# Kernel optimization log

Measured on AMD Instinct MI355X. Metric: run time of the kernel, lower is better.

## Reference

```python
import jax, jax.numpy as jnp
import numpy as np

D = 2048    # d_model (feature_dimm)
H = 8       # n_heads
P = 4       # n_points (n_levels = 1)
NL = 4      # num_encoder_layers
DFF = 2048  # dim_feedforward
BS = 2
T = 2048


def setup_inputs() -> dict:
    key = jax.random.key(0)
    ks = jax.random.split(key, 10)
    s = 0.02
    def w(k, shape):
        return jax.random.normal(k, shape, jnp.float32) * s
    return {
        "src": jax.random.normal(ks[0], (BS, D, T), jnp.float32),
        "mask": jnp.ones((BS, T), dtype=bool),
        "level_embed": w(ks[1], (1, D)),
        "Wo": w(ks[2], (NL, D, H * P)), "bo": jnp.zeros((NL, H * P), jnp.float32),
        "Wa": w(ks[3], (NL, D, H * P)), "ba": jnp.zeros((NL, H * P), jnp.float32),
        "Wv": w(ks[4], (NL, D, D)), "bv": jnp.zeros((NL, D), jnp.float32),
        "Wout": w(ks[5], (NL, D, D)), "bout": jnp.zeros((NL, D), jnp.float32),
        "ln1_g": jnp.ones((NL, D), jnp.float32), "ln1_b": jnp.zeros((NL, D), jnp.float32),
        "W1": w(ks[6], (NL, D, DFF)), "b1": jnp.zeros((NL, DFF), jnp.float32),
        "W2": w(ks[7], (NL, DFF, D)), "b2": jnp.zeros((NL, D), jnp.float32),
        "ln2_g": jnp.ones((NL, D), jnp.float32), "ln2_b": jnp.zeros((NL, D), jnp.float32),
    }


def _layer_norm(x, g, b):
    mu = jnp.mean(x, axis=-1, keepdims=True)
    var = jnp.mean((x - mu) ** 2, axis=-1, keepdims=True)
    return (x - mu) * jax.lax.rsqrt(var + 1e-5) * g + b


def _pos_embed_sine(mask, d):
    # 1D PositionEmbeddingSine, normalize=True, temperature=10000
    bs, t = mask.shape
    emb = jnp.cumsum(mask.astype(jnp.float32), axis=1)
    emb = emb / (emb[:, -1:] + 1e-6) * jnp.float32(2.0 * np.pi)
    dim_t = 10000.0 ** (2.0 * (jnp.arange(d) // 2).astype(jnp.float32) / d)
    pos = emb[:, :, None] / dim_t  # (bs, t, d)
    pos = jnp.stack([jnp.sin(pos[..., 0::2]), jnp.cos(pos[..., 1::2])], axis=3)
    return pos.reshape(bs, t, d)


def _deform_attn(q, src, ref, Wv, bv, Wo, bo, Wa, ba, Wout, bout):
    # 1D multi-scale deformable attention, single level.
    bs, Q, d = q.shape
    T_ = src.shape[1]
    dh = d // H
    value = (src @ Wv + bv).reshape(bs, T_, H, dh)
    off = (q @ Wo + bo).reshape(bs, Q, H, P)
    attn = jax.nn.softmax((q @ Wa + ba).reshape(bs, Q, H, P), axis=-1)
    # normalized sampling locations in [0, 1]
    loc = ref[:, :, 0, 0][:, :, None, None] + off / T_  # (bs, Q, H, P)
    x = loc * T_ - 0.5
    i0 = jnp.floor(x)
    w1 = x - i0
    i0i = i0.astype(jnp.int32)
    i1i = i0i + 1
    v0 = ((i0i >= 0) & (i0i < T_)).astype(jnp.float32)  # zero padding
    v1 = ((i1i >= 0) & (i1i < T_)).astype(jnp.float32)
    i0c = jnp.clip(i0i, 0, T_ - 1)
    i1c = jnp.clip(i1i, 0, T_ - 1)
    vh = value.transpose(0, 2, 1, 3)  # (bs, H, T, dh)
    def gather(idx):  # idx: (bs, Q, H, P) -> (bs, H, Q, P, dh)
        idxh = idx.transpose(0, 2, 1, 3).reshape(bs, H, Q * P)
        g = jnp.take_along_axis(vh, idxh[:, :, :, None], axis=2)
        return g.reshape(bs, H, Q, P, dh)
    w0m = ((1.0 - w1) * v0).transpose(0, 2, 1, 3)  # (bs, H, Q, P)
    w1m = (w1 * v1).transpose(0, 2, 1, 3)
    sampled = gather(i0c) * w0m[..., None] + gather(i1c) * w1m[..., None]
    out = jnp.einsum('bhqp,bhqpd->bhqd', attn.transpose(0, 2, 1, 3), sampled)
    out = out.transpose(0, 2, 1, 3).reshape(bs, Q, d)
    return out @ Wout + bout


def reference(src, mask, level_embed, Wo, bo, Wa, ba, Wv, bv, Wout, bout,
              ln1_g, ln1_b, W1, b1, W2, b2, ln2_g, ln2_b):
    bs, c, t = src.shape
    pos = _pos_embed_sine(mask, c)          # (bs, t, c)
    x = src.transpose(0, 2, 1)              # (bs, t, c)
    lvl_pos = pos + level_embed             # (1, c) broadcasts
    vr = jnp.sum(mask.astype(jnp.float32), axis=1) / t  # valid ratios (bs,)
    ref = jnp.linspace(0.5, t - 0.5, t, dtype=jnp.float32)[None] / (vr[:, None] * t)
    ref = (ref * vr[:, None])[:, :, None, None]  # (bs, t, 1, 1)
    for i in range(NL):
        q = x + lvl_pos
        a = _deform_attn(q, x, ref, Wv[i], bv[i], Wo[i], bo[i], Wa[i], ba[i], Wout[i], bout[i])
        x = _layer_norm(x + a, ln1_g[i], ln1_b[i])
        h = jax.nn.relu(x @ W1[i] + b1[i]) @ W2[i] + b2[i]
        x = _layer_norm(x + h, ln2_g[i], ln2_b[i])
    return (x.transpose(0, 2, 1), mask[:, None])
```

## Files before the change

### kernel.cpp

```cpp
#include <hip/hip_runtime.h>

typedef unsigned int u32;
typedef unsigned short u16;
typedef short s8v __attribute__((ext_vector_type(8)));
typedef float f4v __attribute__((ext_vector_type(4)));

#define D_ 2048
#define T_ 2048
#define BS_ 2
#define H_ 8
#define P_ 4
#define NL_ 4
#define DFF_ 2048
#define LDK_ 2048
#define TBUF 24576

#define AS1 __attribute__((address_space(1)))
#define AS3 __attribute__((address_space(3)))

static __device__ __forceinline__ u16 f2bf(float f) {
    u32 u = __float_as_uint(f);
    u = (u + 0x7FFFu + ((u >> 16) & 1u)) >> 16;
    return (u16)u;
}
static __device__ __forceinline__ float bf2f(u16 v) {
    return __uint_as_float(((u32)v) << 16);
}

__global__ void pos_k(const float* __restrict__ le, u16* __restrict__ posbf) {
    int t = blockIdx.x;
    float scale = ((float)(t + 1)) / (2048.0f + 1e-6f) * 6.283185307179586f;
    for (int d = threadIdx.x; d < D_; d += 256) {
        int k = d >> 1;
        float inv_dt = expf(-(float)k * 0.008994473019508361f);
        float th = scale * inv_dt;
        float v = (d & 1) ? cosf(th) : sinf(th);
        posbf[(size_t)t * D_ + d] = f2bf(v + le[d]);
    }
}

__global__ __launch_bounds__(256) void transpose_src_k(const float* __restrict__ src,
                                                       float* __restrict__ x,
                                                       u16* __restrict__ xbf) {
    __shared__ float tile[64][65];
    int b = blockIdx.z;
    int t0 = blockIdx.x * 64, d0 = blockIdx.y * 64;
    const float* s = src + (size_t)b * D_ * T_;
#pragma unroll
    for (int p = 0; p < 16; ++p) {
        int idx = threadIdx.x + p * 256;
        int r = idx >> 6, c = idx & 63;
        tile[r][c] = s[(size_t)(d0 + r) * T_ + t0 + c];
    }
    __syncthreads();
    float* xb = x + (size_t)b * T_ * D_;
    u16* xbb = xbf + (size_t)b * T_ * D_;
#pragma unroll
    for (int p = 0; p < 16; ++p) {
        int idx = threadIdx.x + p * 256;
        int r = idx >> 6, c = idx & 63;
        float v = tile[c][r];
        size_t o = (size_t)(t0 + r) * D_ + d0 + c;
        xb[o] = v;
        xbb[o] = f2bf(v);
    }
}

__global__ __launch_bounds__(256) void transpose_out_k(const float* __restrict__ x,
                                                       float* __restrict__ outp) {
    __shared__ float tile[64][65];
    int b = blockIdx.z;
    int t0 = blockIdx.x * 64, d0 = blockIdx.y * 64;
    const float* xb = x + (size_t)b * T_ * D_;
#pragma unroll
    for (int p = 0; p < 16; ++p) {
        int idx = threadIdx.x + p * 256;
        int r = idx >> 6, c = idx & 63;
        tile[r][c] = xb[(size_t)(t0 + r) * D_ + d0 + c];
    }
    __syncthreads();
    float* ob = outp + (size_t)b * D_ * T_;
#pragma unroll
    for (int p = 0; p < 16; ++p) {
        int idx = threadIdx.x + p * 256;
        int r = idx >> 6, c = idx & 63;
        ob[(size_t)(d0 + r) * T_ + t0 + c] = tile[c][r];
    }
}

__global__ void mask_out_k(float* __restrict__ outp) {
    int i = blockIdx.x * 256 + threadIdx.x;
    if (i < BS_ * T_) outp[i] = 1.0f;
}

__global__ __launch_bounds__(256) void transpose_cvt4_k(const float* __restrict__ Wv,
                                                        const float* __restrict__ Wout,
                                                        const float* __restrict__ W1,
                                                        const float* __restrict__ W2,
                                                        u16* __restrict__ WtV,
                                                        u16* __restrict__ Wt1,
                                                        u16* __restrict__ Wt2,
                                                        u16* __restrict__ Wt3) {
    __shared__ float tile[64][65];
    int z = blockIdx.z;
    const float* W = (z == 0) ? Wv : (z == 1) ? Wout : (z == 2) ? W1 : W2;
    u16* Wt = (z == 0) ? WtV : (z == 1) ? Wt1 : (z == 2) ? Wt2 : Wt3;
    int k0 = blockIdx.x * 64, n0 = blockIdx.y * 64;
#pragma unroll
    for (int p = 0; p < 16; ++p) {
        int idx = threadIdx.x + p * 256;
        int r = idx >> 6, c = idx & 63;
        tile[r][c] = W[(size_t)(k0 + r) * 2048 + n0 + c];
    }
    __syncthreads();
#pragma unroll
    for (int p = 0; p < 16; ++p) {
        int idx = threadIdx.x + p * 256;
        int r = idx >> 6, c = idx & 63;
        Wt[(size_t)(n0 + r) * 2048 + k0 + c] = f2bf(tile[c][r]);
    }
}

__global__ void build_qtall_k(const float* __restrict__ Wo, const float* __restrict__ Wa,
                              const float* __restrict__ bo, const float* __restrict__ ba,
                              u16* __restrict__ WqtAll, float* __restrict__ bqaAll) {
    int i = blockIdx.x * 256 + threadIdx.x;
    int l = i >> 18;
    int rem = i & 262143;
    int n = rem >> 11, k = rem & 2047;
    float v = 0.f;
    if (n < 32) v = Wo[((size_t)l * 2048 + k) * 32 + n];
    else if (n < 64) v = Wa[((size_t)l * 2048 + k) * 32 + (n - 32)];
    WqtAll[i] = f2bf(v);
    if (i < NL_ * 128) {
        int ll = i >> 7, nn = i & 127;
        float bb = 0.f;
        if (nn < 32) bb = bo[ll * 32 + nn];
        else if (nn < 64) bb = ba[ll * 32 + (nn - 32)];
        bqaAll[i] = bb;
    }
}

static __device__ __forceinline__ void stage6(const u16* __restrict__ As,
                                              const u16* __restrict__ Bs,
                                              u16* lbuf, int w, int k0) {
#pragma unroll
    for (int s = 0; s < 4; ++s) {
        int seg = s * 8 + w;
        __builtin_amdgcn_global_load_lds((AS1 void*)(As + (size_t)(seg * 8) * LDK_ + k0),
                                         (AS3 void*)(lbuf + seg * 512), 16, 0, 0);
    }
#pragma unroll
    for (int s = 0; s < 2; ++s) {
        int seg = s * 8 + w;
        __builtin_amdgcn_global_load_lds((AS1 void*)(Bs + (size_t)(seg * 8) * LDK_ + k0),
                                         (AS3 void*)(lbuf + 16384 + seg * 512), 16, 0, 0);
    }
}

static __device__ __forceinline__ void gemm_core256(const u16* __restrict__ A,
                                                    const u16* __restrict__ Bt,
                                                    int bm, int bn, int kbase, int kext,
                                                    u16* lds, f4v (&acc)[4][4]) {
    int tid = threadIdx.x;
    int w = tid >> 6, lane = tid & 63;
    int quad = lane >> 4, lrow = lane & 15;
    int wr = w >> 1, wc = w & 1;
    int srow = lane >> 3;
    int sg = (lane & 7) ^ srow;
    const u16* As = A + (size_t)(bm * 256 + srow) * LDK_ + kbase + sg * 8;
    const u16* Bs = Bt + (size_t)(bn * 128 + srow) * LDK_ + kbase + sg * 8;
    int nt = kext >> 6;

    stage6(As, Bs, lds, w, 0);
    stage6(As, Bs, lds + TBUF, w, 64);
    int cur = 0, nxt = 2;
    for (int t = 0; t < nt; ++t) {
        if (t != nt - 1)
            asm volatile("s_waitcnt vmcnt(6)" ::: "memory");
        else
            asm volatile("s_waitcnt vmcnt(0)" ::: "memory");
        __builtin_amdgcn_s_barrier();
        __builtin_amdgcn_sched_barrier(0);
        if (t + 2 < nt) stage6(As, Bs, lds + nxt * TBUF, w, (t + 2) << 6);
        const u16* lA = lds + cur * TBUF;
        const u16* lB = lA + 16384;

        s8v af[2][2], bfr[4][2];
#pragma unroll
        for (int i = 0; i < 2; ++i) {
            int r = wr * 64 + i * 16 + lrow;
#pragma unroll
            for (int c = 0; c < 2; ++c)
                af[i][c] = *(const s8v*)&lA[r * 64 + (((c * 4 + quad) ^ (r & 7)) * 8)];
        }
#pragma unroll
        for (int j = 0; j < 4; ++j) {
            int r = wc * 64 + j * 16 + lrow;
#pragma unroll
            for (int c = 0; c < 2; ++c)
                bfr[j][c] = *(const s8v*)&lB[r * 64 + (((c * 4 + quad) ^ (r & 7)) * 8)];
        }
        __builtin_amdgcn_s_setprio(1);
#pragma unroll
        for (int c = 0; c < 2; ++c)
#pragma unroll
            for (int i = 0; i < 2; ++i)
#pragma unroll
                for (int j = 0; j < 4; ++j)
                    acc[i][j] = __builtin_amdgcn_mfma_f32_16x16x32_bf16(af[i][c], bfr[j][c],
                                                                       acc[i][j], 0, 0, 0);
        __builtin_amdgcn_s_setprio(0);
#pragma unroll
        for (int i = 0; i < 2; ++i) {
            int r = wr * 64 + (i + 2) * 16 + lrow;
#pragma unroll
            for (int c = 0; c < 2; ++c)
                af[i][c] = *(const s8v*)&lA[r * 64 + (((c * 4 + quad) ^ (r & 7)) * 8)];
        }
        __builtin_amdgcn_s_setprio(1);
#pragma unroll
        for (int c = 0; c < 2; ++c)
#pragma unroll
            for (int i = 0; i < 2; ++i)
#pragma unroll
                for (int j = 0; j < 4; ++j)
                    acc[i + 2][j] = __builtin_amdgcn_mfma_f32_16x16x32_bf16(af[i][c], bfr[j][c],
                                                                            acc[i + 2][j], 0, 0, 0);
        __builtin_amdgcn_s_setprio(0);
        cur = (cur == 2) ? 0 : cur + 1;
        nxt = (nxt == 2) ? 0 : nxt + 1;
    }
}

static __device__ __forceinline__ void store_bf_ep(u16* __restrict__ C, int N, int row0, int col0,
                                                   const float* __restrict__ bias, int relu,
                                                   f4v (&acc)[4][4], int quad, int lrow) {
#pragma unroll
    for (int j = 0; j < 4; ++j) {
        int col = col0 + j * 16 + lrow;
        float bcol = bias[col];
#pragma unroll
        for (int i = 0; i < 4; ++i) {
            int rbase = row0 + i * 16 + quad * 4;
#pragma unroll
            for (int r = 0; r < 4; ++r) {
                float vv = acc[i][j][r] + bcol;
                if (relu) vv = fmaxf(vv, 0.f);
                C[(size_t)(rbase + r) * N + col] = f2bf(vv);
            }
        }
    }
}

__global__ __launch_bounds__(512, 2) void gemm_f32_256(const u16* __restrict__ A,
                                                       const u16* __restrict__ Bt,
                                                       const float* __restrict__ bias,
                                                       float* __restrict__ C, int N) {
    __shared__ u16 lds[3 * TBUF];
    f4v acc[4][4] = {};
    gemm_core256(A, Bt, blockIdx.x, blockIdx.y, 0, LDK_, lds, acc);
    int tid = threadIdx.x, w = tid >> 6, lane = tid & 63;
    int quad = lane >> 4, lrow = lane & 15, wr = w >> 1, wc = w & 1;
    int row0 = blockIdx.x * 256 + wr * 64;
    int col0 = blockIdx.y * 128 + wc * 64;
#pragma unroll
    for (int j = 0; j < 4; ++j) {
        int col = col0 + j * 16 + lrow;
        float bcol = bias[col];
#pragma unroll
        for (int i = 0; i < 4; ++i) {
            int rbase = row0 + i * 16 + quad * 4;
#pragma unroll
            for (int r = 0; r < 4; ++r)
                C[(size_t)(rbase + r) * N + col] = acc[i][j][r] + bcol;
        }
    }
}

__global__ __launch_bounds__(512, 2) void gemm_bf256(const u16* __restrict__ A,
                                                     const u16* __restrict__ Bt,
                                                     const float* __restrict__ bias,
                                                     u16* __restrict__ C,
                                                     int N, int relu) {
    __shared__ u16 lds[3 * TBUF];
    f4v acc[4][4] = {};
    int f = blockIdx.x;
    int xcd = f & 7, local = f >> 3;
    int bm = xcd * 2 + (local & 1);
    int bn = local >> 1;
    gemm_core256(A, Bt, bm, bn, 0, LDK_, lds, acc);
    int tid = threadIdx.x, w = tid >> 6, lane = tid & 63;
    int quad = lane >> 4, lrow = lane & 15, wr = w >> 1, wc = w & 1;
    store_bf_ep(C, N, bm * 256 + wr * 64, bn * 128 + wc * 64, bias, relu, acc, quad, lrow);
}

__global__ __launch_bounds__(512, 2) void gemm_vq256(const u16* __restrict__ A,
                                                     const u16* __restrict__ WtV,
                                                     const u16* __restrict__ WtQ,
                                                     const float* __restrict__ bv,
                                                     u16* __restrict__ value,
                                                     float* __restrict__ smp) {
    __shared__ u16 lds[3 * TBUF];
    f4v acc[4][4] = {};
    int f = blockIdx.x;
    int xcd = f & 7, local = f >> 3;
    int tid = threadIdx.x, w = tid >> 6, lane = tid & 63;
    int quad = lane >> 4, lrow = lane & 15, wr = w >> 1, wc = w & 1;
    if (local < 32) {
        int bm = xcd * 2 + (local & 1);
        int bn = local >> 1;
        gemm_core256(A, WtV, bm, bn, 0, LDK_, lds, acc);
        store_bf_ep(value, 2048, bm * 256 + wr * 64, bn * 128 + wc * 64, bv, 0, acc, quad, lrow);
    } else {
        int j2 = local - 32;
        int bm = xcd * 2 + (j2 & 1);
        int ks = j2 >> 1;
        gemm_core256(A, WtQ, bm, 0, ks * 512, 512, lds, acc);
        if (wc == 0) {
            int row0 = bm * 256 + wr * 64;
            float* sp = smp + (size_t)ks * (4096 * 64);
#pragma unroll
            for (int j = 0; j < 4; ++j) {
                int col = j * 16 + lrow;
#pragma unroll
                for (int i = 0; i < 4; ++i) {
                    int rbase = row0 + i * 16 + quad * 4;
#pragma unroll
                    for (int r = 0; r < 4; ++r)
                        sp[(size_t)(rbase + r) * 64 + col] = acc[i][j][r];
                }
            }
        }
    }
}

__global__ __launch_bounds__(256) void sampler_k(const u16* __restrict__ value,
                                                 const float* __restrict__ smp,
                                                 const float* __restrict__ Ppos,
                                                 int loff,
                                                 u16* __restrict__ abf) {
    int bq = blockIdx.x;
    int qi = bq & (T_ - 1);
    int b = bq >> 11;
    __shared__ float s[64];
    if (threadIdx.x < 64) {
        float v = Ppos[(size_t)qi * (NL_ * 128) + loff + threadIdx.x];
        v += smp[(size_t)bq * 64 + threadIdx.x];
        v += smp[262144 + (size_t)bq * 64 + threadIdx.x];
        v += smp[2 * 262144 + (size_t)bq * 64 + threadIdx.x];
        v += smp[3 * 262144 + (size_t)bq * 64 + threadIdx.x];
        s[threadIdx.x] = v;
    }
    __syncthreads();
    int c = threadIdx.x;
    const u16* vb = value + (size_t)b * T_ * D_;
    u16* ob = abf + (size_t)bq * D_;
    for (int h = 0; h < H_; ++h) {
        float l0 = s[32 + h * 4 + 0], l1 = s[32 + h * 4 + 1];
        float l2 = s[32 + h * 4 + 2], l3 = s[32 + h * 4 + 3];
        float mx = fmaxf(fmaxf(l0, l1), fmaxf(l2, l3));
        float e0 = __expf(l0 - mx), e1 = __expf(l1 - mx);
        float e2 = __expf(l2 - mx), e3 = __expf(l3 - mx);
        float inv = 1.f / (e0 + e1 + e2 + e3);
        float at[4] = {e0 * inv, e1 * inv, e2 * inv, e3 * inv};
        float o = 0.f;
#pragma unroll
        for (int p = 0; p < 4; ++p) {
            float xp = (float)qi + s[h * 4 + p];
            float fl = floorf(xp);
            float w1 = xp - fl;
            int i0 = (int)fl;
            int i1 = i0 + 1;
            float w0m = (i0 >= 0 && i0 < T_) ? (1.f - w1) : 0.f;
            float w1m = (i1 >= 0 && i1 < T_) ? w1 : 0.f;
            int i0c = min(max(i0, 0), T_ - 1);
            int i1c = min(max(i1, 0), T_ - 1);
            o += at[p] * (w0m * bf2f(vb[(size_t)i0c * D_ + h * 256 + c]) +
                          w1m * bf2f(vb[(size_t)i1c * D_ + h * 256 + c]));
        }
        ob[h * 256 + c] = f2bf(o);
    }
}

__global__ __launch_bounds__(256) void resid_ln_k(const float* __restrict__ xin,
                                                  const u16* __restrict__ res,
                                                  const float* __restrict__ g,
                                                  const float* __restrict__ be,
                                                  float* __restrict__ xout,
                                                  u16* __restrict__ xbf) {
    int row = blockIdx.x;
    int base = threadIdx.x * 8;
    const float* xr = xin + (size_t)row * D_ + base;
    const u16* rr = res + (size_t)row * D_ + base;
    f4v x0 = *(const f4v*)xr;
    f4v x1 = *(const f4v*)(xr + 4);
    s8v rv = *(const s8v*)rr;
    float v[8];
#pragma unroll
    for (int i = 0; i < 4; ++i) v[i] = x0[i] + bf2f((u16)rv[i]);
#pragma unroll
    for (int i = 0; i < 4; ++i) v[4 + i] = x1[i] + bf2f((u16)rv[4 + i]);
    float s = 0.f, ss = 0.f;
#pragma unroll
    for (int i = 0; i < 8; ++i) { s += v[i]; ss += v[i] * v[i]; }
#pragma unroll
    for (int o = 32; o > 0; o >>= 1) {
        s += __shfl_down(s, o, 64);
        ss += __shfl_down(ss, o, 64);
    }
    __shared__ float w1s[4], w2s[4];
    int wid = threadIdx.x >> 6, lane = threadIdx.x & 63;
    if (lane == 0) { w1s[wid] = s; w2s[wid] = ss; }
    __syncthreads();
    s = w1s[0] + w1s[1] + w1s[2] + w1s[3];
    ss = w2s[0] + w2s[1] + w2s[2] + w2s[3];
    float mu = s * (1.f / 2048.f);
    float var = ss * (1.f / 2048.f) - mu * mu;
    float rinv = rsqrtf(var + 1e-5f);
    f4v g0 = *(const f4v*)(g + base);
    f4v g1 = *(const f4v*)(g + base + 4);
    f4v b0 = *(const f4v*)(be + base);
    f4v b1 = *(const f4v*)(be + base + 4);
    f4v y0, y1;
    s8v yb;
#pragma unroll
    for (int i = 0; i < 4; ++i) {
        float y = (v[i] - mu) * rinv * g0[i] + b0[i];
        y0[i] = y;
        yb[i] = (short)f2bf(y);
    }
#pragma unroll
    for (int i = 0; i < 4; ++i) {
        float y = (v[4 + i] - mu) * rinv * g1[i] + b1[i];
        y1[i] = y;
        yb[4 + i] = (short)f2bf(y);
    }
    float* xo = xout + (size_t)row * D_ + base;
    *(f4v*)xo = y0;
    *(f4v*)(xo + 4) = y1;
    *(s8v*)(xbf + (size_t)row * D_ + base) = yb;
}

extern "C" void kernel_launch(void* const* d_in, const int* in_sizes, int n_in,
                              void* d_out, int out_size, void* d_ws, size_t ws_size,
                              hipStream_t stream) {
    const float* src = (const float*)d_in[0];
    const float* level_embed = (const float*)d_in[2];
    const float* Wo = (const float*)d_in[3];
    const float* bo = (const float*)d_in[4];
    const float* Wa = (const float*)d_in[5];
    const float* ba = (const float*)d_in[6];
    const float* Wv = (const float*)d_in[7];
    const float* bv = (const float*)d_in[8];
    const float* Wout = (const float*)d_in[9];
    const float* bout = (const float*)d_in[10];
    const float* ln1_g = (const float*)d_in[11];
    const float* ln1_b = (const float*)d_in[12];
    const float* W1 = (const float*)d_in[13];
    const float* b1 = (const float*)d_in[14];
    const float* W2 = (const float*)d_in[15];
    const float* b2 = (const float*)d_in[16];
    const float* ln2_g = (const float*)d_in[17];
    const float* ln2_b = (const float*)d_in[18];
    float* outp = (float*)d_out;

    char* p = (char*)d_ws;
    auto alloc = [&](size_t bytes) {
        char* r = p;
        p += (bytes + 255) & ~(size_t)255;
        return r;
    };
    const size_t BTD = (size_t)BS_ * T_ * D_;
    float* B_x = (float*)alloc(BTD * 4);
    u16* B_xbf = (u16*)alloc(BTD * 2);
    u16* B_res = (u16*)alloc(BTD * 2);
    u16* B_val = (u16*)alloc(BTD * 2);
    u16* B_h = (u16*)alloc(BTD * 2);
    float* B_smp = (float*)alloc((size_t)4 * 4096 * 64 * 4);
    u16* B_posbf = (u16*)alloc((size_t)T_ * D_ * 2);
    u16* WtV = (u16*)alloc((size_t)D_ * D_ * 2);
    u16* Wt1 = (u16*)alloc((size_t)D_ * D_ * 2);
    u16* Wt2 = (u16*)alloc((size_t)D_ * DFF_ * 2);
    u16* Wt3 = (u16*)alloc((size_t)DFF_ * D_ * 2);
    u16* WqtAll = (u16*)alloc((size_t)NL_ * 128 * D_ * 2);
    float* bqaAll = (float*)alloc(NL_ * 128 * 4);
    float* Ppos = (float*)alloc((size_t)T_ * NL_ * 128 * 4);

    const int M = BS_ * T_;
    dim3 blk(256);
    dim3 gT(T_ / 64, D_ / 64, BS_);
    dim3 gW4(D_ / 64, D_ / 64, 4);

    pos_k<<<T_, blk, 0, stream>>>(level_embed, B_posbf);
    transpose_src_k<<<gT, blk, 0, stream>>>(src, B_x, B_xbf);
    build_qtall_k<<<(NL_ * 128 * D_) / 256, blk, 0, stream>>>(Wo, Wa, bo, ba, WqtAll, bqaAll);
    gemm_f32_256<<<dim3(T_ / 256, NL_ * 128 / 128), dim3(512), 0, stream>>>(
        B_posbf, WqtAll, bqaAll, Ppos, NL_ * 128);

    for (int l = 0; l < NL_; ++l) {
        transpose_cvt4_k<<<gW4, blk, 0, stream>>>(
            Wv + (size_t)l * D_ * D_, Wout + (size_t)l * D_ * D_,
            W1 + (size_t)l * D_ * DFF_, W2 + (size_t)l * DFF_ * D_,
            WtV, Wt1, Wt2, Wt3);

        gemm_vq256<<<320, dim3(512), 0, stream>>>(B_xbf, WtV, WqtAll + (size_t)l * 128 * D_,
                                                  bv + l * D_, B_val, B_smp);
        sampler_k<<<M, blk, 0, stream>>>(B_val, B_smp, Ppos, l * 128, B_h);
        gemm_bf256<<<256, dim3(512), 0, stream>>>(B_h, Wt1, bout + l * D_, B_res, D_, 0);
        resid_ln_k<<<M, blk, 0, stream>>>(B_x, B_res, ln1_g + l * D_, ln1_b + l * D_, B_x, B_xbf);
        gemm_bf256<<<256, dim3(512), 0, stream>>>(B_xbf, Wt2, b1 + l * DFF_, B_h, DFF_, 1);
        gemm_bf256<<<256, dim3(512), 0, stream>>>(B_h, Wt3, b2 + l * D_, B_res, D_, 0);
        resid_ln_k<<<M, blk, 0, stream>>>(B_x, B_res, ln2_g + l * D_, ln2_b + l * D_, B_x, B_xbf);
    }

    transpose_out_k<<<gT, blk, 0, stream>>>(B_x, outp);
    mask_out_k<<<(BS_ * T_ + 255) / 256, blk, 0, stream>>>(outp + BTD);
}
```

Before: 1.187 ms.

## Interleave prefetch stores with MFMA quarter-phases and reorder VQ block dispatch

The GEMM main loop is split into four MFMA quarters (2x2 sub-tiles). LDS fragment reads and the global_load_lds prefetch of the next-next tile are spread across these phases, separated by barriers, so global-to-LDS traffic overlaps matrix math instead of being issued all at once at loop start. The fused value/offset GEMM kernel also dispatches the smaller split-K query blocks first and the value blocks after, which changes scheduling and tail balance. The extra barriers per iteration add sync overhead and can stall waves.

```diff
diff --git a/kernel.cpp b/kernel.cpp
--- a/kernel.cpp
+++ b/kernel.cpp
@@ -174,60 +174,110 @@
 
     stage6(As, Bs, lds, w, 0);
     stage6(As, Bs, lds + TBUF, w, 64);
+    asm volatile("s_waitcnt vmcnt(6)" ::: "memory");
+    __builtin_amdgcn_s_barrier();
     int cur = 0, nxt = 2;
     for (int t = 0; t < nt; ++t) {
-        if (t != nt - 1)
-            asm volatile("s_waitcnt vmcnt(6)" ::: "memory");
-        else
-            asm volatile("s_waitcnt vmcnt(0)" ::: "memory");
-        __builtin_amdgcn_s_barrier();
-        __builtin_amdgcn_sched_barrier(0);
-        if (t + 2 < nt) stage6(As, Bs, lds + nxt * TBUF, w, (t + 2) << 6);
         const u16* lA = lds + cur * TBUF;
         const u16* lB = lA + 16384;
-
-        s8v af[2][2], bfr[4][2];
-#pragma unroll
-        for (int i = 0; i < 2; ++i) {
-            int r = wr * 64 + i * 16 + lrow;
-#pragma unroll
-            for (int c = 0; c < 2; ++c)
-                af[i][c] = *(const s8v*)&lA[r * 64 + (((c * 4 + quad) ^ (r & 7)) * 8)];
-        }
-#pragma unroll
-        for (int j = 0; j < 4; ++j) {
-            int r = wc * 64 + j * 16 + lrow;
-#pragma unroll
-            for (int c = 0; c < 2; ++c)
-                bfr[j][c] = *(const s8v*)&lB[r * 64 + (((c * 4 + quad) ^ (r & 7)) * 8)];
-        }
+        u16* pbuf = lds + nxt * TBUF;
+        bool pf = (t + 2) < nt;
+        int k2 = (t + 2) << 6;
+
+        auto rdA = [&](s8v (&dst)[2][2], int mh) {
+#pragma unroll
+            for (int i = 0; i < 2; ++i) {
+                int r = wr * 64 + (mh * 2 + i) * 16 + lrow;
+#pragma unroll
+                for (int c = 0; c < 2; ++c)
+                    dst[i][c] = *(const s8v*)&lA[r * 64 + (((c * 4 + quad) ^ (r & 7)) * 8)];
+            }
+        };
+        auto rdB = [&](s8v (&dst)[2][2], int nh) {
+#pragma unroll
+            for (int j = 0; j < 2; ++j) {
+                int r = wc * 64 + (nh * 2 + j) * 16 + lrow;
+#pragma unroll
+                for (int c = 0; c < 2; ++c)
+                    dst[j][c] = *(const s8v*)&lB[r * 64 + (((c * 4 + quad) ^ (r & 7)) * 8)];
+            }
+        };
+        auto stA = [&](int s) {
+            int seg = s * 8 + w;
+            __builtin_amdgcn_global_load_lds((AS1 void*)(As + (size_t)(seg * 8) * LDK_ + k2),
+                                             (AS3 void*)(pbuf + seg * 512), 16, 0, 0);
+        };
+        auto stB = [&](int s) {
+            int seg = s * 8 + w;
+            __builtin_amdgcn_global_load_lds((AS1 void*)(Bs + (size_t)(seg * 8) * LDK_ + k2),
+                                             (AS3 void*)(pbuf + 16384 + seg * 512), 16, 0, 0);
+        };
+
+        s8v af[2][2], b0f[2][2], b1f[2][2];
+        rdA(af, 0);
+        rdB(b0f, 0);
+        if (pf) { stA(0); stA(1); }
+        __builtin_amdgcn_sched_barrier(0);
+        __builtin_amdgcn_s_barrier();
         __builtin_amdgcn_s_setprio(1);
 #pragma unroll
         for (int c = 0; c < 2; ++c)
 #pragma unroll
             for (int i = 0; i < 2; ++i)
 #pragma unroll
-                for (int j = 0; j < 4; ++j)
-                    acc[i][j] = __builtin_amdgcn_mfma_f32_16x16x32_bf16(af[i][c], bfr[j][c],
+                for (int j = 0; j < 2; ++j)
+                    acc[i][j] = __builtin_amdgcn_mfma_f32_16x16x32_bf16(af[i][c], b0f[j][c],
                                                                        acc[i][j], 0, 0, 0);
         __builtin_amdgcn_s_setprio(0);
-#pragma unroll
-        for (int i = 0; i < 2; ++i) {
-            int r = wr * 64 + (i + 2) * 16 + lrow;
-#pragma unroll
-            for (int c = 0; c < 2; ++c)
-                af[i][c] = *(const s8v*)&lA[r * 64 + (((c * 4 + quad) ^ (r & 7)) * 8)];
-        }
+        __builtin_amdgcn_sched_barrier(0);
+        __builtin_amdgcn_s_barrier();
+        rdB(b1f, 1);
+        if (pf) { stA(2); stA(3); }
+        __builtin_amdgcn_sched_barrier(0);
+        __builtin_amdgcn_s_barrier();
         __builtin_amdgcn_s_setprio(1);
 #pragma unroll
         for (int c = 0; c < 2; ++c)
 #pragma unroll
             for (int i = 0; i < 2; ++i)
 #pragma unroll
-                for (int j = 0; j < 4; ++j)
-                    acc[i + 2][j] = __builtin_amdgcn_mfma_f32_16x16x32_bf16(af[i][c], bfr[j][c],
+                for (int j = 0; j < 2; ++j)
+                    acc[i][j + 2] = __builtin_amdgcn_mfma_f32_16x16x32_bf16(af[i][c], b1f[j][c],
+                                                                            acc[i][j + 2], 0, 0, 0);
+        __builtin_amdgcn_s_setprio(0);
+        __builtin_amdgcn_sched_barrier(0);
+        __builtin_amdgcn_s_barrier();
+        rdA(af, 1);
+        if (pf) stB(0);
+        __builtin_amdgcn_sched_barrier(0);
+        __builtin_amdgcn_s_barrier();
+        __builtin_amdgcn_s_setprio(1);
+#pragma unroll
+        for (int c = 0; c < 2; ++c)
+#pragma unroll
+            for (int i = 0; i < 2; ++i)
+#pragma unroll
+                for (int j = 0; j < 2; ++j)
+                    acc[i + 2][j] = __builtin_amdgcn_mfma_f32_16x16x32_bf16(af[i][c], b0f[j][c],
                                                                             acc[i + 2][j], 0, 0, 0);
         __builtin_amdgcn_s_setprio(0);
+        __builtin_amdgcn_sched_barrier(0);
+        __builtin_amdgcn_s_barrier();
+        if (pf) stB(1);
+        __builtin_amdgcn_s_setprio(1);
+#pragma unroll
+        for (int c = 0; c < 2; ++c)
+#pragma unroll
+            for (int i = 0; i < 2; ++i)
+#pragma unroll
+                for (int j = 0; j < 2; ++j)
+                    acc[i + 2][j + 2] = __builtin_amdgcn_mfma_f32_16x16x32_bf16(af[i][c], b1f[j][c],
+                                                                               acc[i + 2][j + 2], 0, 0, 0);
+        __builtin_amdgcn_s_setprio(0);
+        if (pf) asm volatile("s_waitcnt vmcnt(6)" ::: "memory");
+        else    asm volatile("s_waitcnt vmcnt(0)" ::: "memory");
+        __builtin_amdgcn_sched_barrier(0);
+        __builtin_amdgcn_s_barrier();
         cur = (cur == 2) ? 0 : cur + 1;
         nxt = (nxt == 2) ? 0 : nxt + 1;
     }
@@ -304,16 +354,17 @@
     __shared__ u16 lds[3 * TBUF];
     f4v acc[4][4] = {};
     int f = blockIdx.x;
-    int xcd = f & 7, local = f >> 3;
     int tid = threadIdx.x, w = tid >> 6, lane = tid & 63;
     int quad = lane >> 4, lrow = lane & 15, wr = w >> 1, wc = w & 1;
-    if (local < 32) {
+    if (f >= 64) {
+        int g = f - 64;
+        int xcd = g & 7, local = g >> 3;
         int bm = xcd * 2 + (local & 1);
         int bn = local >> 1;
         gemm_core256(A, WtV, bm, bn, 0, LDK_, lds, acc);
         store_bf_ep(value, 2048, bm * 256 + wr * 64, bn * 128 + wc * 64, bv, 0, acc, quad, lrow);
     } else {
-        int j2 = local - 32;
+        int xcd = f & 7, j2 = f >> 3;
         int bm = xcd * 2 + (j2 & 1);
         int ks = j2 >> 1;
         gemm_core256(A, WtQ, bm, 0, ks * 512, 512, lds, acc);
```

After: 1.267 ms. +6.7%, slower.

## Split query-projection GEMM into 8 K-slices and vectorize sampler per head

Applied to the files above, without the earlier changes.

The fused value/query GEMM kernel now splits the small query-projection GEMM into 8 K-slices of 256 instead of 4 of 512. Those short blocks are scheduled first (low block indices), ahead of the 256 value-GEMM tiles, to balance load across the 384-block launch. The sampler accumulates 8 partial sums. Each sampler thread now handles one head and 8 contiguous channels with 16-byte vector loads, replacing a per-head loop of scalar bf16 loads. The cost is more partial-sum traffic and a larger scratch buffer.

```diff
diff --git a/kernel.cpp b/kernel.cpp
--- a/kernel.cpp
+++ b/kernel.cpp
@@ -304,19 +304,19 @@
     __shared__ u16 lds[3 * TBUF];
     f4v acc[4][4] = {};
     int f = blockIdx.x;
-    int xcd = f & 7, local = f >> 3;
     int tid = threadIdx.x, w = tid >> 6, lane = tid & 63;
     int quad = lane >> 4, lrow = lane & 15, wr = w >> 1, wc = w & 1;
-    if (local < 32) {
+    if (f >= 128) {
+        int g = f - 128;
+        int xcd = g & 7, local = g >> 3;
         int bm = xcd * 2 + (local & 1);
         int bn = local >> 1;
         gemm_core256(A, WtV, bm, bn, 0, LDK_, lds, acc);
         store_bf_ep(value, 2048, bm * 256 + wr * 64, bn * 128 + wc * 64, bv, 0, acc, quad, lrow);
     } else {
-        int j2 = local - 32;
-        int bm = xcd * 2 + (j2 & 1);
-        int ks = j2 >> 1;
-        gemm_core256(A, WtQ, bm, 0, ks * 512, 512, lds, acc);
+        int ks = f >> 4;
+        int bm = f & 15;
+        gemm_core256(A, WtQ, bm, 0, ks * 256, 256, lds, acc);
         if (wc == 0) {
             int row0 = bm * 256 + wr * 64;
             float* sp = smp + (size_t)ks * (4096 * 64);
@@ -346,41 +346,47 @@
     __shared__ float s[64];
     if (threadIdx.x < 64) {
         float v = Ppos[(size_t)qi * (NL_ * 128) + loff + threadIdx.x];
-        v += smp[(size_t)bq * 64 + threadIdx.x];
-        v += smp[262144 + (size_t)bq * 64 + threadIdx.x];
-        v += smp[2 * 262144 + (size_t)bq * 64 + threadIdx.x];
-        v += smp[3 * 262144 + (size_t)bq * 64 + threadIdx.x];
+        const float* sp = smp + (size_t)bq * 64 + threadIdx.x;
+#pragma unroll
+        for (int ks = 0; ks < 8; ++ks) v += sp[(size_t)ks * (4096 * 64)];
         s[threadIdx.x] = v;
     }
     __syncthreads();
-    int c = threadIdx.x;
-    const u16* vb = value + (size_t)b * T_ * D_;
-    u16* ob = abf + (size_t)bq * D_;
-    for (int h = 0; h < H_; ++h) {
-        float l0 = s[32 + h * 4 + 0], l1 = s[32 + h * 4 + 1];
-        float l2 = s[32 + h * 4 + 2], l3 = s[32 + h * 4 + 3];
-        float mx = fmaxf(fmaxf(l0, l1), fmaxf(l2, l3));
-        float e0 = __expf(l0 - mx), e1 = __expf(l1 - mx);
-        float e2 = __expf(l2 - mx), e3 = __expf(l3 - mx);
-        float inv = 1.f / (e0 + e1 + e2 + e3);
-        float at[4] = {e0 * inv, e1 * inv, e2 * inv, e3 * inv};
-        float o = 0.f;
-#pragma unroll
-        for (int p = 0; p < 4; ++p) {
-            float xp = (float)qi + s[h * 4 + p];
-            float fl = floorf(xp);
-            float w1 = xp - fl;
-            int i0 = (int)fl;
-            int i1 = i0 + 1;
-            float w0m = (i0 >= 0 && i0 < T_) ? (1.f - w1) : 0.f;
-            float w1m = (i1 >= 0 && i1 < T_) ? w1 : 0.f;
-            int i0c = min(max(i0, 0), T_ - 1);
-            int i1c = min(max(i1, 0), T_ - 1);
-            o += at[p] * (w0m * bf2f(vb[(size_t)i0c * D_ + h * 256 + c]) +
-                          w1m * bf2f(vb[(size_t)i1c * D_ + h * 256 + c]));
-        }
-        ob[h * 256 + c] = f2bf(o);
-    }
+    int head = threadIdx.x >> 5;
+    int c8 = (threadIdx.x & 31) * 8;
+    const u16* vb = value + (size_t)b * T_ * D_ + head * 256 + c8;
+
+    float l0 = s[32 + head * 4 + 0], l1 = s[32 + head * 4 + 1];
+    float l2 = s[32 + head * 4 + 2], l3 = s[32 + head * 4 + 3];
+    float mx = fmaxf(fmaxf(l0, l1), fmaxf(l2, l3));
+    float e0 = __expf(l0 - mx), e1 = __expf(l1 - mx);
+    float e2 = __expf(l2 - mx), e3 = __expf(l3 - mx);
+    float inv = 1.f / (e0 + e1 + e2 + e3);
+    float at[4] = {e0 * inv, e1 * inv, e2 * inv, e3 * inv};
+
+    float o[8] = {};
+#pragma unroll
+    for (int p = 0; p < 4; ++p) {
+        float xp = (float)qi + s[head * 4 + p];
+        float fl = floorf(xp);
+        float w1 = xp - fl;
+        int i0 = (int)fl;
+        int i1 = i0 + 1;
+        float w0m = (i0 >= 0 && i0 < T_) ? (1.f - w1) : 0.f;
+        float w1m = (i1 >= 0 && i1 < T_) ? w1 : 0.f;
+        int i0c = min(max(i0, 0), T_ - 1);
+        int i1c = min(max(i1, 0), T_ - 1);
+        s8v v0 = *(const s8v*)(vb + (size_t)i0c * D_);
+        s8v v1 = *(const s8v*)(vb + (size_t)i1c * D_);
+        float a = at[p];
+#pragma unroll
+        for (int e = 0; e < 8; ++e)
+            o[e] += a * (w0m * bf2f((u16)v0[e]) + w1m * bf2f((u16)v1[e]));
+    }
+    s8v ov;
+#pragma unroll
+    for (int e = 0; e < 8; ++e) ov[e] = (short)f2bf(o[e]);
+    *(s8v*)(abf + (size_t)bq * D_ + head * 256 + c8) = ov;
 }
 
 __global__ __launch_bounds__(256) void resid_ln_k(const float* __restrict__ xin,
@@ -477,7 +483,7 @@
     u16* B_res = (u16*)alloc(BTD * 2);
     u16* B_val = (u16*)alloc(BTD * 2);
     u16* B_h = (u16*)alloc(BTD * 2);
-    float* B_smp = (float*)alloc((size_t)4 * 4096 * 64 * 4);
+    float* B_smp = (float*)alloc((size_t)8 * 4096 * 64 * 4);
     u16* B_posbf = (u16*)alloc((size_t)T_ * D_ * 2);
     u16* WtV = (u16*)alloc((size_t)D_ * D_ * 2);
     u16* Wt1 = (u16*)alloc((size_t)D_ * D_ * 2);
@@ -504,7 +510,7 @@
             W1 + (size_t)l * D_ * DFF_, W2 + (size_t)l * DFF_ * D_,
             WtV, Wt1, Wt2, Wt3);
 
-        gemm_vq256<<<320, dim3(512), 0, stream>>>(B_xbf, WtV, WqtAll + (size_t)l * 128 * D_,
+        gemm_vq256<<<384, dim3(512), 0, stream>>>(B_xbf, WtV, WqtAll + (size_t)l * 128 * D_,
                                                   bv + l * D_, B_val, B_smp);
         sampler_k<<<M, blk, 0, stream>>>(B_val, B_smp, Ppos, l * 128, B_h);
         gemm_bf256<<<256, dim3(512), 0, stream>>>(B_h, Wt1, bout + l * D_, B_res, D_, 0);
```

Result: no change. 1.172 ms (-1.3%).
